# Optimization experiments

Measured on AMD Instinct MI355X. Metric: run time of the kernel, lower is better.

The kernel has to match this reference:

```python
import jax, jax.numpy as jnp
import numpy as np

N, T, L = 4, 2048, 2048
DQIN, DFEAT, DQK, DV = 32, 34, 64, 64  # modality feat=34 -> V input = 34-2 = 32, K input = last col


def _sorted_timeline(k, shape):
    return jnp.sort(jax.random.uniform(k, shape, jnp.float32) * 100.0, axis=-1)


def setup_inputs() -> dict:
    key = jax.random.key(0)
    ks = jax.random.split(key, 32)
    inp = {}
    inp["ref_data"] = jax.random.normal(ks[0], (N, 1, T, DQIN), jnp.float32)
    inp["ref_t"] = _sorted_timeline(ks[1], (N, 1, T))
    inp["m1_data"] = jax.random.normal(ks[2], (N, 1, L, DFEAT), jnp.float32)
    inp["m1_t"] = _sorted_timeline(ks[3], (N, 1, L))
    inp["m2_data"] = jax.random.normal(ks[4], (N, 1, L, DFEAT), jnp.float32)
    inp["m2_t"] = _sorted_timeline(ks[5], (N, 1, L))
    inp["m3_data"] = jax.random.normal(ks[6], (N, 1, L, DFEAT), jnp.float32)
    inp["m3_t"] = _sorted_timeline(ks[7], (N, 1, L))
    # shared W_Q (bias=False): d_q_in -> d_qk
    inp["Wq"] = jax.random.normal(ks[8], (DQIN, DQK), jnp.float32) / np.sqrt(DQIN)
    # per-modality params: W_K: 1 -> d_qk (with bias), W_V: (DFEAT-2) -> d_v (with bias), log-temperature
    for i, m in enumerate(["1", "2", "3"]):
        b = 9 + 4 * i
        inp["Wk" + m] = jax.random.normal(ks[b], (1, DQK), jnp.float32)
        inp["bk" + m] = jax.random.normal(ks[b + 1], (DQK,), jnp.float32) * 0.02
        inp["Wv" + m] = jax.random.normal(ks[b + 2], (DFEAT - 2, DV), jnp.float32) / np.sqrt(DFEAT - 2)
        inp["bv" + m] = jax.random.normal(ks[b + 3], (DV,), jnp.float32) * 0.02
        inp["log_tau" + m] = jnp.zeros((), jnp.float32)  # log(init_tau=1)
    return inp


def _unimodal(Q, ref_t, data, t, Wk, bk, Wv, bv, log_tau):
    # K path: last feature column through linear, then feature_map_k = [1, -x]
    Kr = data[..., -1:] @ Wk + bk                                   # (N,1,L,DQK)
    K = jnp.concatenate([jnp.ones(Kr.shape[:-1] + (1,), Kr.dtype), -Kr], axis=-1)  # (N,1,L,DQK+1)
    V = data[..., :-2] @ Wv + bv                                    # (N,1,L,DV)
    tau = jnp.exp(log_tau)
    # gaussian weight: -(Q.K)^2 / tau
    S = -jnp.square(jnp.einsum('nhtc,nhlc->nhtl', Q, K)) / tau       # (N,1,T,L)
    mask = (ref_t[..., :, None] >= t[..., None, :]).astype(S.dtype)  # (N,1,T,L)
    A = jax.nn.softmax(S * mask, axis=-1) * mask
    return jnp.einsum('nhtl,nhlc->nhtc', A, V)                       # (N,1,T,DV)


def reference(ref_data, ref_t, m1_data, m1_t, m2_data, m2_t, m3_data, m3_t,
              Wq, Wk1, bk1, Wv1, bv1, log_tau1, Wk2, bk2, Wv2, bv2, log_tau2,
              Wk3, bk3, Wv3, bv3, log_tau3):
    # compute_Q (qk_type='time'): Q = add_one(W_Q(ref_data)) -> append ones column
    Qr = jnp.einsum('nhtd,dk->nhtk', ref_data, Wq)
    Q = jnp.concatenate([Qr, jnp.ones(Qr.shape[:-1] + (1,), Qr.dtype)], axis=-1)  # (N,1,T,DQK+1)
    y1 = _unimodal(Q, ref_t, m1_data, m1_t, Wk1, bk1, Wv1, bv1, log_tau1)
    y2 = _unimodal(Q, ref_t, m2_data, m2_t, Wk2, bk2, Wv2, bv2, log_tau2)
    y3 = _unimodal(Q, ref_t, m3_data, m3_t, Wk3, bk3, Wv3, bv3, log_tau3)
    # original returns dict {m1: y1, m2: y2, m3: y3}; stacked here (3,N,1,T,DV)
    return jnp.stack([y1, y2, y3], axis=0)
```

## Files before the change

kernel.cpp:

```cpp
#include <hip/hip_runtime.h>

namespace {

typedef unsigned int uint;
typedef unsigned short ushort_t;
typedef __attribute__((ext_vector_type(8))) short bf16x8;
typedef __attribute__((ext_vector_type(4))) float f32x4;

constexpr int N = 4, T = 2048, L = 2048;
constexpr int DQIN = 32, DQK = 64;

constexpr int VI_SZ = 3 * N * 64 * L;
constexpr int X_SZ = 3 * N * L;
constexpr int A_SZ = 3 * N * T;

union PK8 { int i[4]; bf16x8 s; };

__global__ __launch_bounds__(256) void mm_prep(
    const float* __restrict__ ref_data, const float* __restrict__ ref_t,
    const float* __restrict__ d1, const float* __restrict__ t1,
    const float* __restrict__ d2, const float* __restrict__ t2,
    const float* __restrict__ d3, const float* __restrict__ t3,
    const float* __restrict__ Wq,
    const float* __restrict__ Wk1, const float* __restrict__ bk1,
    const float* __restrict__ Wv1, const float* __restrict__ bv1, const float* __restrict__ lt1,
    const float* __restrict__ Wk2, const float* __restrict__ bk2,
    const float* __restrict__ Wv2, const float* __restrict__ bv2, const float* __restrict__ lt2,
    const float* __restrict__ Wk3, const float* __restrict__ bk3,
    const float* __restrict__ Wv3, const float* __restrict__ bv3, const float* __restrict__ lt3,
    float* __restrict__ Aq, float* __restrict__ Gq, int* __restrict__ Cq,
    ushort_t* __restrict__ VI, float* __restrict__ X) {
  const int b = blockIdx.x;
  const int tid = threadIdx.x;

  if (b < 96) {
    const int m = b >> 5;
    const int idx = (b & 31) * 256 + tid;
    __shared__ float sWq[DQIN * DQK];
    __shared__ float sWk[DQK];
    __shared__ float sbk[DQK];
    const float* Wk = (m == 0) ? Wk1 : (m == 1 ? Wk2 : Wk3);
    const float* bk = (m == 0) ? bk1 : (m == 1 ? bk2 : bk3);
    const float* lt = (m == 0) ? lt1 : (m == 1 ? lt2 : lt3);
    for (int i = tid; i < DQIN * DQK; i += 256) sWq[i] = Wq[i];
    if (tid < DQK) { sWk[tid] = Wk[tid]; sbk[tid] = bk[tid]; }
    __syncthreads();
    float x[DQIN];
    const float* rp = ref_data + idx * DQIN;
#pragma unroll
    for (int i = 0; i < DQIN; i++) x[i] = rp[i];
    float qr[DQK];
#pragma unroll
    for (int j = 0; j < DQK; j += 4) {
      float4 acc4 = make_float4(0.f, 0.f, 0.f, 0.f);
#pragma unroll
      for (int i = 0; i < DQIN; i++) {
        const float4 w = *(const float4*)&sWq[i * DQK + j];
        acc4.x = fmaf(x[i], w.x, acc4.x);
        acc4.y = fmaf(x[i], w.y, acc4.y);
        acc4.z = fmaf(x[i], w.z, acc4.z);
        acc4.w = fmaf(x[i], w.w, acc4.w);
      }
      qr[j] = acc4.x; qr[j + 1] = acc4.y; qr[j + 2] = acc4.z; qr[j + 3] = acc4.w;
    }
    const float rs = __expf(-0.5f * lt[0]);
    float g = 0.f, h = 0.f;
#pragma unroll
    for (int j = 1; j < DQK; j++) {
      g = fmaf(qr[j], sWk[j - 1], g);
      h = fmaf(qr[j], sbk[j - 1], h);
    }
    g += sWk[DQK - 1];
    h += sbk[DQK - 1];
    Aq[m * (N * T) + idx] = (qr[0] - h) * rs;
    Gq[m * (N * T) + idx] = g * rs;
  } else if (b < 192) {
    const int sidx = (b - 96) * 256 + tid;
    const int m = sidx >> 13;
    const int nt = sidx & 8191;
    const int n = nt >> 11;
    const float rt = ref_t[nt];
    const float* tml = ((m == 0) ? t1 : (m == 1 ? t2 : t3)) + n * L;
    int lo = 0, hi = L;
    while (lo < hi) {
      const int mid = (lo + hi) >> 1;
      if (tml[mid] <= rt) lo = mid + 1; else hi = mid;
    }
    Cq[m * 8192 + nt] = lo;
  } else {
    const int vb = b - 192;
    const int mn = vb >> 5;
    const int m = mn >> 2, n = mn & 3;
    const int lseg0 = (vb & 31) * 64;
    const float* dm = (m == 0) ? d1 : (m == 1 ? d2 : d3);
    const float* Wv = (m == 0) ? Wv1 : (m == 1 ? Wv2 : Wv3);
    const float* bv = (m == 0) ? bv1 : (m == 1 ? bv2 : bv3);
    const int cdim = tid & 63;
    const int qq = tid >> 6;
    const int l0 = lseg0 + qq * 16;

    float Wc[32];
#pragma unroll
    for (int i = 0; i < 32; i++) Wc[i] = Wv[i * 64 + cdim];
    const float bvc = bv[cdim];

    uint hi16[16], lo16[16];
#pragma unroll 4
    for (int k = 0; k < 16; k++) {
      const float* dp = dm + (size_t)(n * L + l0 + k) * 34;
      float acc = bvc;
#pragma unroll
      for (int i = 0; i < 32; i++) acc = fmaf(dp[i], Wc[i], acc);
      uint u = __float_as_uint(acc);
      uint h = (u + 0x7fffu + ((u >> 16) & 1u)) & 0xffff0000u;
      float res = acc - __uint_as_float(h);
      uint ul = __float_as_uint(res);
      uint hl = (ul + 0x7fffu + ((ul >> 16) & 1u)) >> 16;
      hi16[k] = h >> 16;
      lo16[k] = hl;
    }
    int pkh[8], pkl[8];
#pragma unroll
    for (int p = 0; p < 8; p++) {
      pkh[p] = (int)(hi16[2 * p] | (hi16[2 * p + 1] << 16));
      pkl[p] = (int)(lo16[2 * p] | (lo16[2 * p + 1] << 16));
    }
    ushort_t* dst = VI + (size_t)(mn * 64 + cdim) * (2 * L) + (l0 >> 3) * 16;
    *(int4*)dst = make_int4(pkh[0], pkh[1], pkh[2], pkh[3]);
    *(int4*)(dst + 8) = make_int4(pkl[0], pkl[1], pkl[2], pkl[3]);
    *(int4*)(dst + 16) = make_int4(pkh[4], pkh[5], pkh[6], pkh[7]);
    *(int4*)(dst + 24) = make_int4(pkl[4], pkl[5], pkl[6], pkl[7]);

    if (tid < 64) {
      const int l = lseg0 + tid;
      X[mn * L + l] = dm[(size_t)(n * L + l) * 34 + 33];
    }
  }
}

__device__ inline void stage_chunk(ushort_t* dstbuf, const ushort_t* VIb, int ch,
                                   int w, int lane) {
#pragma unroll
  for (int i = 0; i < 8; i++) {
    const int n = (w * 8 + i) * 64 + lane;
    const int lr = n >> 5;
    const int slot = n & 31;
    const int u = (slot - lr) & 31;
    const ushort_t* src = VIb + (size_t)lr * 4096 + ch * 256 + u * 8;
    __builtin_amdgcn_global_load_lds(
        (const __attribute__((address_space(1))) void*)src,
        (__attribute__((address_space(3))) void*)(dstbuf + (w * 8 + i) * 512),
        16, 0, 0);
  }
}

__global__ __launch_bounds__(128, 2) void mm_attn_main(
    const ushort_t* __restrict__ VI, const float* __restrict__ X,
    const float* __restrict__ Aq, const float* __restrict__ Gq, const int* __restrict__ Cq,
    float* __restrict__ out) {
  __shared__ ushort_t sbuf[2][8192];
  __shared__ float sx[2048];

  const int b = blockIdx.x;
  const int mn = b % 12;
  const int j = b / 12;
  const int pj = 63 - j;

  const int tid = threadIdx.x;
  const int lane = tid & 63;
  const int w = tid >> 6;
  const int q = lane >> 4;
  const int m16 = lane & 15;

  const int rg = pj * 2 + w;
  const int tbase = mn * T + rg * 16;

  const int c = Cq[tbase + m16];
  const int cmax = __shfl(c, 15, 64);
  const int cmin = __shfl(c, 0, 64);
  const int nch = (cmax + 127) >> 7;

  const int cB = Cq[mn * T + (pj * 2 + 1) * 16 + 15];
  const int nchB = (cB + 127) >> 7;

  const float a = Aq[tbase + m16];
  const float g = Gq[tbase + m16];

  f32x4 acc[4];
#pragma unroll
  for (int i = 0; i < 4; i++) acc[i] = (f32x4){0.f, 0.f, 0.f, 0.f};
  float z = 0.f;

  const ushort_t* VIh0 = VI + (size_t)(mn * 64) * 4096;
  const ushort_t* VIh1 = VI + (size_t)(mn * 64 + 32) * 4096;
  const float* xg = X + mn * L;

  int oh[2][4], ol[2][4];
#pragma unroll
  for (int ct = 0; ct < 2; ct++) {
#pragma unroll
    for (int kk = 0; kk < 4; kk++) {
      const int lr = ct * 16 + m16;
      const int uh = (kk * 4 + q) * 2;
      oh[ct][kk] = lr * 256 + (((uh + 0) + lr) & 31) * 8;
      ol[ct][kk] = lr * 256 + (((uh + 1) + lr) & 31) * 8;
    }
  }

#pragma unroll
  for (int i = 0; i < 4; i++) {
    const float* src = xg + (w * 4 + i) * 256 + lane * 4;
    __builtin_amdgcn_global_load_lds(
        (const __attribute__((address_space(1))) void*)src,
        (__attribute__((address_space(3))) void*)(sx + (w * 4 + i) * 256),
        16, 0, 0);
  }
  stage_chunk(sbuf[0], VIh0, 0, w, lane);
  __syncthreads();

  for (int ch = 0; ch < nchB; ch++) {
    stage_chunk(sbuf[1], VIh1, ch, w, lane);

    bf16x8 sh[4], sl[4];
    if (ch < nch) {
      const int base = ch << 7;
      const ushort_t* buf = sbuf[0];
      const bool inter = (base + 128 <= cmin);
#pragma unroll
      for (int kk = 0; kk < 4; kk++) {
        const int k0 = base + kk * 32 + q * 8;
        const float4 xa = *(const float4*)&sx[k0];
        const float4 xb = *(const float4*)&sx[k0 + 4];
        const float xs[8] = {xa.x, xa.y, xa.z, xa.w, xb.x, xb.y, xb.z, xb.w};
        float wv[8];
        if (inter) {
#pragma unroll
          for (int jj = 0; jj < 8; jj++) {
            const float d = fmaf(-g, xs[jj], a);
            wv[jj] = __expf(-d * d);
            z += wv[jj];
          }
        } else {
#pragma unroll
          for (int jj = 0; jj < 8; jj++) {
            const float d = fmaf(-g, xs[jj], a);
            const float e = __expf(-d * d);
            wv[jj] = (k0 + jj < c) ? e : 0.f;
            z += wv[jj];
          }
        }
        PK8 ph, pl;
#pragma unroll
        for (int p2 = 0; p2 < 4; p2++) {
          const uint u0 = __float_as_uint(wv[2 * p2]);
          const uint u1 = __float_as_uint(wv[2 * p2 + 1]);
          const uint h0 = u0 & 0xffff0000u, h1 = u1 & 0xffff0000u;
          const float l0f = wv[2 * p2] - __uint_as_float(h0);
          const float l1f = wv[2 * p2 + 1] - __uint_as_float(h1);
          ph.i[p2] = (int)((h0 >> 16) | h1);
          pl.i[p2] = (int)((__float_as_uint(l0f) >> 16) | (__float_as_uint(l1f) & 0xffff0000u));
        }
        sh[kk] = ph.s;
        sl[kk] = pl.s;
#pragma unroll
        for (int ct = 0; ct < 2; ct++) {
          const bf16x8 bh = *(const bf16x8*)(buf + oh[ct][kk]);
          const bf16x8 bl = *(const bf16x8*)(buf + ol[ct][kk]);
          acc[ct] = __builtin_amdgcn_mfma_f32_16x16x32_bf16(sh[kk], bh, acc[ct], 0, 0, 0);
          acc[ct] = __builtin_amdgcn_mfma_f32_16x16x32_bf16(sh[kk], bl, acc[ct], 0, 0, 0);
          acc[ct] = __builtin_amdgcn_mfma_f32_16x16x32_bf16(sl[kk], bh, acc[ct], 0, 0, 0);
        }
      }
    }
    __syncthreads();

    if (ch + 1 < nchB) stage_chunk(sbuf[0], VIh0, ch + 1, w, lane);

    if (ch < nch) {
      const ushort_t* buf = sbuf[1];
#pragma unroll
      for (int kk = 0; kk < 4; kk++) {
#pragma unroll
        for (int ct = 0; ct < 2; ct++) {
          const bf16x8 bh = *(const bf16x8*)(buf + oh[ct][kk]);
          const bf16x8 bl = *(const bf16x8*)(buf + ol[ct][kk]);
          acc[2 + ct] = __builtin_amdgcn_mfma_f32_16x16x32_bf16(sh[kk], bh, acc[2 + ct], 0, 0, 0);
          acc[2 + ct] = __builtin_amdgcn_mfma_f32_16x16x32_bf16(sh[kk], bl, acc[2 + ct], 0, 0, 0);
          acc[2 + ct] = __builtin_amdgcn_mfma_f32_16x16x32_bf16(sl[kk], bh, acc[2 + ct], 0, 0, 0);
        }
      }
    }
    __syncthreads();
  }

  z += __shfl_xor(z, 16, 64);
  z += __shfl_xor(z, 32, 64);

#pragma unroll
  for (int rr = 0; rr < 4; rr++) {
    const int row = q * 4 + rr;
    const float zr = __shfl(z, row, 64);
    const int cr = __shfl(c, row, 64);
    const float inv = 1.0f / (zr + (float)(L - cr));
#pragma unroll
    for (int hh = 0; hh < 2; hh++) {
#pragma unroll
      for (int ct = 0; ct < 2; ct++) {
        out[(size_t)(tbase + row) * 64 + hh * 32 + ct * 16 + m16] =
            acc[hh * 2 + ct][rr] * inv;
      }
    }
  }
}

}

extern "C" void kernel_launch(void* const* d_in, const int* in_sizes, int n_in,
                              void* d_out, int out_size, void* d_ws, size_t ws_size,
                              hipStream_t stream) {
  const float* ref_data = (const float*)d_in[0];
  const float* ref_t = (const float*)d_in[1];
  const float* m1_data = (const float*)d_in[2];
  const float* m1_t = (const float*)d_in[3];
  const float* m2_data = (const float*)d_in[4];
  const float* m2_t = (const float*)d_in[5];
  const float* m3_data = (const float*)d_in[6];
  const float* m3_t = (const float*)d_in[7];
  const float* Wq = (const float*)d_in[8];
  const float* Wk1 = (const float*)d_in[9];
  const float* bk1 = (const float*)d_in[10];
  const float* Wv1 = (const float*)d_in[11];
  const float* bv1 = (const float*)d_in[12];
  const float* lt1 = (const float*)d_in[13];
  const float* Wk2 = (const float*)d_in[14];
  const float* bk2 = (const float*)d_in[15];
  const float* Wv2 = (const float*)d_in[16];
  const float* bv2 = (const float*)d_in[17];
  const float* lt2 = (const float*)d_in[18];
  const float* Wk3 = (const float*)d_in[19];
  const float* bk3 = (const float*)d_in[20];
  const float* Wv3 = (const float*)d_in[21];
  const float* bv3 = (const float*)d_in[22];
  const float* lt3 = (const float*)d_in[23];

  float* ws = (float*)d_ws;
  ushort_t* VI = (ushort_t*)ws;
  float* Xw = ws + VI_SZ;
  float* Aq = Xw + X_SZ;
  float* Gq = Aq + A_SZ;
  int* Cq = (int*)(Gq + A_SZ);

  mm_prep<<<dim3(576), dim3(256), 0, stream>>>(
      ref_data, ref_t, m1_data, m1_t, m2_data, m2_t, m3_data, m3_t, Wq,
      Wk1, bk1, Wv1, bv1, lt1, Wk2, bk2, Wv2, bv2, lt2, Wk3, bk3, Wv3, bv3, lt3,
      Aq, Gq, Cq, VI, Xw);
  mm_attn_main<<<dim3(12 * 64), dim3(128), 0, stream>>>(
      VI, Xw, Aq, Gq, Cq, (float*)d_out);
}
```

Measured before the change: 156.8 us.

## Halve chunk size and prefetch next chunk with vmcnt-gated double buffering

Shrinks the staged key chunk from 128 to 64 columns and splits the LDS into four half-buffers, so the next chunk's two V halves load while the current chunk computes. Full __syncthreads are replaced by explicit s_waitcnt vmcnt counts plus raw s_barrier, so outstanding async LDS loads can stay in flight across iterations. The aim is to hide global-to-LDS latency and cut masked-tail waste by using finer chunks. In exchange it doubles the number of loop iterations and barriers, and it depends on hand-counted vmcnt values, which are fragile if the compiler emits other memory ops.

```diff
diff --git a/kernel.cpp b/kernel.cpp
--- a/kernel.cpp
+++ b/kernel.cpp
@@ -138,18 +138,18 @@
   }
 }
 
-__device__ inline void stage_chunk(ushort_t* dstbuf, const ushort_t* VIb, int ch,
-                                   int w, int lane) {
-#pragma unroll
-  for (int i = 0; i < 8; i++) {
-    const int n = (w * 8 + i) * 64 + lane;
-    const int lr = n >> 5;
-    const int slot = n & 31;
-    const int u = (slot - lr) & 31;
-    const ushort_t* src = VIb + (size_t)lr * 4096 + ch * 256 + u * 8;
+__device__ inline void stage_half(ushort_t* dstbuf, const ushort_t* VIb, int ch,
+                                  int w, int lane) {
+#pragma unroll
+  for (int i = 0; i < 4; i++) {
+    const int n = (w * 4 + i) * 64 + lane;
+    const int lr = n >> 4;
+    const int slot = n & 15;
+    const int u = (slot - lr) & 15;
+    const ushort_t* src = VIb + (size_t)lr * 4096 + ch * 128 + u * 8;
     __builtin_amdgcn_global_load_lds(
         (const __attribute__((address_space(1))) void*)src,
-        (__attribute__((address_space(3))) void*)(dstbuf + (w * 8 + i) * 512),
+        (__attribute__((address_space(3))) void*)(dstbuf + (w * 4 + i) * 512),
         16, 0, 0);
   }
 }
@@ -158,7 +158,7 @@
     const ushort_t* __restrict__ VI, const float* __restrict__ X,
     const float* __restrict__ Aq, const float* __restrict__ Gq, const int* __restrict__ Cq,
     float* __restrict__ out) {
-  __shared__ ushort_t sbuf[2][8192];
+  __shared__ ushort_t sbuf[4][4096];
   __shared__ float sx[2048];
 
   const int b = blockIdx.x;
@@ -178,10 +178,10 @@
   const int c = Cq[tbase + m16];
   const int cmax = __shfl(c, 15, 64);
   const int cmin = __shfl(c, 0, 64);
-  const int nch = (cmax + 127) >> 7;
+  const int nch = (cmax + 63) >> 6;
 
   const int cB = Cq[mn * T + (pj * 2 + 1) * 16 + 15];
-  const int nchB = (cB + 127) >> 7;
+  const int nchB = (cB + 63) >> 6;
 
   const float a = Aq[tbase + m16];
   const float g = Gq[tbase + m16];
@@ -195,15 +195,15 @@
   const ushort_t* VIh1 = VI + (size_t)(mn * 64 + 32) * 4096;
   const float* xg = X + mn * L;
 
-  int oh[2][4], ol[2][4];
+  int oh[2][2], ol[2][2];
 #pragma unroll
   for (int ct = 0; ct < 2; ct++) {
 #pragma unroll
-    for (int kk = 0; kk < 4; kk++) {
+    for (int kk = 0; kk < 2; kk++) {
       const int lr = ct * 16 + m16;
       const int uh = (kk * 4 + q) * 2;
-      oh[ct][kk] = lr * 256 + (((uh + 0) + lr) & 31) * 8;
-      ol[ct][kk] = lr * 256 + (((uh + 1) + lr) & 31) * 8;
+      oh[ct][kk] = lr * 128 + (((uh + 0) + lr) & 15) * 8;
+      ol[ct][kk] = lr * 128 + (((uh + 1) + lr) & 15) * 8;
     }
   }
 
@@ -215,19 +215,29 @@
         (__attribute__((address_space(3))) void*)(sx + (w * 4 + i) * 256),
         16, 0, 0);
   }
-  stage_chunk(sbuf[0], VIh0, 0, w, lane);
-  __syncthreads();
+  stage_half(sbuf[0], VIh0, 0, w, lane);
+  stage_half(sbuf[1], VIh1, 0, w, lane);
 
   for (int ch = 0; ch < nchB; ch++) {
-    stage_chunk(sbuf[1], VIh1, ch, w, lane);
-
-    bf16x8 sh[4], sl[4];
+    const bool lastc = (ch + 1 == nchB);
+    const int bp = (ch & 1) << 1;
+
+    if (!lastc) {
+      stage_half(sbuf[bp ^ 2], VIh0, ch + 1, w, lane);
+      asm volatile("s_waitcnt vmcnt(8)" ::: "memory");
+    } else {
+      asm volatile("s_waitcnt vmcnt(4)" ::: "memory");
+    }
+    __builtin_amdgcn_s_barrier();
+    asm volatile("" ::: "memory");
+
+    bf16x8 sh[2], sl[2];
     if (ch < nch) {
-      const int base = ch << 7;
-      const ushort_t* buf = sbuf[0];
-      const bool inter = (base + 128 <= cmin);
-#pragma unroll
-      for (int kk = 0; kk < 4; kk++) {
+      const int base = ch << 6;
+      const ushort_t* buf = sbuf[bp];
+      const bool inter = (base + 64 <= cmin);
+#pragma unroll
+      for (int kk = 0; kk < 2; kk++) {
         const int k0 = base + kk * 32 + q * 8;
         const float4 xa = *(const float4*)&sx[k0];
         const float4 xb = *(const float4*)&sx[k0 + 4];
@@ -272,14 +282,20 @@
         }
       }
     }
-    __syncthreads();
-
-    if (ch + 1 < nchB) stage_chunk(sbuf[0], VIh0, ch + 1, w, lane);
+
+    if (!lastc) {
+      stage_half(sbuf[(bp ^ 2) + 1], VIh1, ch + 1, w, lane);
+      asm volatile("s_waitcnt vmcnt(8)" ::: "memory");
+    } else {
+      asm volatile("s_waitcnt vmcnt(0)" ::: "memory");
+    }
+    __builtin_amdgcn_s_barrier();
+    asm volatile("" ::: "memory");
 
     if (ch < nch) {
-      const ushort_t* buf = sbuf[1];
-#pragma unroll
-      for (int kk = 0; kk < 4; kk++) {
+      const ushort_t* buf = sbuf[bp + 1];
+#pragma unroll
+      for (int kk = 0; kk < 2; kk++) {
 #pragma unroll
         for (int ct = 0; ct < 2; ct++) {
           const bf16x8 bh = *(const bf16x8*)(buf + oh[ct][kk]);
@@ -290,7 +306,6 @@
         }
       }
     }
-    __syncthreads();
   }
 
   z += __shfl_xor(z, 16, 64);
```

Result: slower. 165.5 us (+5.5%).
